# Kernel optimization log

Hardware: AMD Instinct MI355X
Metric: run time of the kernel (lower is better)

Reference implementation:

```python
import jax, jax.numpy as jnp
import numpy as np

B, T, I, H = 64, 2048, 64, 128


def setup_inputs() -> dict:
    key = jax.random.key(0)
    ks = jax.random.split(key, 6)
    std = 1.0 / np.sqrt(H)
    return {
        "x": jax.random.normal(ks[0], (B, T, I), dtype=jnp.float32),
        "h0": jax.random.normal(ks[1], (B, H), dtype=jnp.float32),
        "W": jax.random.uniform(ks[2], (H, I), dtype=jnp.float32, minval=-std, maxval=std),
        "U": jax.random.uniform(ks[3], (H, H), dtype=jnp.float32, minval=-std, maxval=std),
        "b_ih": jax.random.uniform(ks[4], (H,), dtype=jnp.float32, minval=-std, maxval=std),
        "b_hh": jax.random.uniform(ks[5], (H,), dtype=jnp.float32, minval=-std, maxval=std),
    }


def reference(x, h0, W, U, b_ih, b_hh):
    # Precompute the input projection for all timesteps in one big GEMM:
    # xw[b,t,h] = W x_t + b_ih + b_hh  (biases folded in once)
    xw = jnp.einsum("bti,hi->bth", x, W) + b_ih + b_hh  # [B,T,H]
    xw_t = jnp.swapaxes(xw, 0, 1)  # [T,B,H] for scan over time

    def step(h, xt):
        # vanilla tanh RNN cell: h' = tanh(W x + U h + b_ih + b_hh)
        h_new = jnp.tanh(xt + h @ U.T)
        return h_new, h_new

    h_last, ys = jax.lax.scan(step, h0, xw_t)  # ys: [T,B,H]
    output = jnp.swapaxes(ys, 0, 1)  # batch_first -> [B,T,H]
    return output, h_last
```

## Files before the change

kernel.cpp:

```cpp
#include <hip/hip_runtime.h>


#define RNN_B 64
#define RNN_T 2048
#define RNN_I 64
#define RNN_H 128
#define CH    32
#define NCH   (RNN_T / CH)

__device__ __forceinline__ float fast_tanh(float x) {
  float e = __builtin_amdgcn_exp2f(x * 2.885390081777927f);
  return 1.0f - 2.0f * __builtin_amdgcn_rcpf(e + 1.0f);
}

template <int CTRL>
__device__ __forceinline__ float dpp_add(float s) {
  int o = __builtin_amdgcn_mov_dpp(__float_as_int(s), CTRL, 0xF, 0xF, true);
  return s + __int_as_float(o);
}

__device__ __forceinline__ void fma4(float4& a, const float4 u, const float4 h) {
  a.x = fmaf(u.x, h.x, a.x);
  a.y = fmaf(u.y, h.y, a.y);
  a.z = fmaf(u.z, h.z, a.z);
  a.w = fmaf(u.w, h.w, a.w);
}

__device__ __forceinline__ float hsum(const float4 a) {
  return (a.x + a.y) + (a.z + a.w);
}

__device__ __forceinline__ void pin4(float4& v) {
  asm volatile("" : "+v"(v.x), "+v"(v.y), "+v"(v.z), "+v"(v.w));
}

__global__ __launch_bounds__(256, 2) void rnn_xw_gemm(
    const float* __restrict__ x, const float* __restrict__ W,
    const float* __restrict__ b_ih, const float* __restrict__ b_hh,
    float* __restrict__ xw) {
  const int tid = threadIdx.x;
  const int g   = tid >> 2;
  const int q   = tid & 3;

  float4 w[2][4];
#pragma unroll
  for (int r = 0; r < 2; ++r) {
    const float4* Wr = (const float4*)(W + (2 * g + r) * RNN_I + 16 * q);
#pragma unroll
    for (int m = 0; m < 4; ++m) { w[r][m] = Wr[m]; pin4(w[r][m]); }
  }
  const int row_own = 2 * g + (q & 1);
  const float bias  = b_ih[row_own] + b_hh[row_own];

  __shared__ __align__(16) float4 xs[64 * 16];
  const long rbase = (long)blockIdx.x * 64;
  const float4* xg = (const float4*)(x + rbase * RNN_I);
#pragma unroll
  for (int jj = 0; jj < 4; ++jj) xs[tid + 256 * jj] = xg[tid + 256 * jj];
  __syncthreads();

  for (int r = 0; r < 64; ++r) {
    const float4* xr = xs + r * 16 + q * 4;
    float4 a0 = {0, 0, 0, 0}, a1 = {0, 0, 0, 0};
#pragma unroll
    for (int m = 0; m < 4; ++m) {
      const float4 xv = xr[m];
      fma4(a0, w[0][m], xv);
      fma4(a1, w[1][m], xv);
    }
    float s0 = hsum(a0), s1 = hsum(a1);
    s0 = dpp_add<0xB1>(s0); s0 = dpp_add<0x4E>(s0);
    s1 = dpp_add<0xB1>(s1); s1 = dpp_add<0x4E>(s1);
    const float own = (q & 1) ? s1 : s0;
    if (q < 2)
      xw[(rbase + r) * RNN_H + row_own] = own + bias;
  }
}

__global__ __launch_bounds__(512, 2) void rnn_scan(
    const float* xw,
    float* out, float* __restrict__ hlast,
    const float* __restrict__ h0, const float* __restrict__ U) {
  const int b     = blockIdx.x;
  const int tid   = threadIdx.x;
  const int g     = tid >> 3;
  const int j     = tid & 7;
  const int r_own = 2 * g + (j & 1);

  __shared__ __align__(16) float hbuf0[8 * 20];
  __shared__ __align__(16) float hbuf1[8 * 20];
  __shared__ __align__(16) float xbuf[CH * RNN_H];
  __shared__ __align__(16) float obuf[CH * RNN_H];

  float4 u[2][4];
#pragma unroll
  for (int r = 0; r < 2; ++r) {
    const float4* Ur = (const float4*)(U + (2 * g + r) * RNN_H + 16 * j);
#pragma unroll
    for (int m = 0; m < 4; ++m) { u[r][m] = Ur[m]; pin4(u[r][m]); }
  }

  if (tid < RNN_H)
    hbuf0[(tid >> 4) * 20 + (tid & 15)] = h0[b * RNN_H + tid];

  const int hoff = (r_own >> 4) * 20 + (r_own & 15);
  const long base   = (long)b * RNN_T * RNN_H;
  const float4* xw4 = (const float4*)(xw + base);
  float4* out4      = (float4*)(out + base);
  float4* xb4       = (float4*)xbuf;
  const float4* ob4 = (const float4*)obuf;

  float4 p0 = xw4[tid], p1 = xw4[tid + 512];

  auto step = [&](const float* src, float* dst, int tc) {
    const float xv = xbuf[tc * RNN_H + r_own];
    const float4* hp = (const float4*)(src + 20 * j);
    float4 a0 = {0, 0, 0, 0}, a1 = {0, 0, 0, 0};
#pragma unroll
    for (int m = 0; m < 4; ++m) {
      const float4 hv = hp[m];
      fma4(a0, u[0][m], hv);
      fma4(a1, u[1][m], hv);
    }
    float s0 = hsum(a0), s1 = hsum(a1);
    s0 = dpp_add<0xB1>(s0); s0 = dpp_add<0x4E>(s0); s0 = dpp_add<0x141>(s0);
    s1 = dpp_add<0xB1>(s1); s1 = dpp_add<0x4E>(s1); s1 = dpp_add<0x141>(s1);
    const float own = (j & 1) ? s1 : s0;
    const float val = fast_tanh(own + xv);
    if (j < 2) {
      dst[hoff] = val;
    } else if ((j & 6) == 4) {
      obuf[tc * RNN_H + r_own] = val;
    }
    __syncthreads();
  };

  for (int c = 0; c < NCH; ++c) {
    xb4[tid] = p0; xb4[tid + 512] = p1;
    if (c + 1 < NCH) {
      const float4* nx = xw4 + (long)(c + 1) * 1024;
      p0 = nx[tid]; p1 = nx[tid + 512];
    }
    if (c > 0) {
      out4[(long)(c - 1) * 1024 + tid]       = ob4[tid];
      out4[(long)(c - 1) * 1024 + tid + 512] = ob4[tid + 512];
    }
    __syncthreads();

    for (int tc = 0; tc < CH; tc += 2) {
      step(hbuf0, hbuf1, tc);
      step(hbuf1, hbuf0, tc + 1);
    }
  }

  out4[(long)(NCH - 1) * 1024 + tid]       = ob4[tid];
  out4[(long)(NCH - 1) * 1024 + tid + 512] = ob4[tid + 512];
  if (tid < RNN_H)
    hlast[b * RNN_H + tid] = hbuf0[(tid >> 4) * 20 + (tid & 15)];
}

extern "C" void kernel_launch(void* const* d_in, const int* in_sizes, int n_in,
                              void* d_out, int out_size, void* d_ws, size_t ws_size,
                              hipStream_t stream) {
  const float* x    = (const float*)d_in[0];
  const float* h0   = (const float*)d_in[1];
  const float* W    = (const float*)d_in[2];
  const float* U    = (const float*)d_in[3];
  const float* b_ih = (const float*)d_in[4];
  const float* b_hh = (const float*)d_in[5];

  float* out   = (float*)d_out;
  float* hlast = out + (long)RNN_B * RNN_T * RNN_H;

  rnn_xw_gemm<<<(RNN_B * RNN_T) / 64, 256, 0, stream>>>(x, W, b_ih, b_hh, out);
  rnn_scan<<<RNN_B, 512, 0, stream>>>(out, out, hlast, h0, U);
}
```

Baseline: 800.8 us.

## Repartition RNN matvec to 4 rows x 8 columns per thread with 16-lane DPP reduction

Both kernels now give each thread 4 output rows and an 8-element column slice instead of 2 rows and 16 columns. Each step reads fewer LDS h values per thread, and the dot products use serial FMA chains. The cross-lane reduction grows to 4 DPP adds over 16 lanes for each of 4 partial sums. The scan also loads the next step's xw from shared memory ahead of the barrier to keep it off the critical path, and the padded h-buffer layout changes to fit the new read pattern. The trade is more DPP reduction work per step against shorter LDS reads and FMA chains.

```diff
diff --git a/kernel.cpp b/kernel.cpp
--- a/kernel.cpp
+++ b/kernel.cpp
@@ -19,19 +19,17 @@
   return s + __int_as_float(o);
 }
 
-__device__ __forceinline__ void fma4(float4& a, const float4 u, const float4 h) {
-  a.x = fmaf(u.x, h.x, a.x);
-  a.y = fmaf(u.y, h.y, a.y);
-  a.z = fmaf(u.z, h.z, a.z);
-  a.w = fmaf(u.w, h.w, a.w);
-}
-
-__device__ __forceinline__ float hsum(const float4 a) {
-  return (a.x + a.y) + (a.z + a.w);
-}
-
-__device__ __forceinline__ void pin4(float4& v) {
-  asm volatile("" : "+v"(v.x), "+v"(v.y), "+v"(v.z), "+v"(v.w));
+__device__ __forceinline__ float dot8(const float4 u0, const float4 u1,
+                                      const float4 h0, const float4 h1) {
+  float s = u0.x * h0.x;
+  s = fmaf(u0.y, h0.y, s);
+  s = fmaf(u0.z, h0.z, s);
+  s = fmaf(u0.w, h0.w, s);
+  s = fmaf(u1.x, h1.x, s);
+  s = fmaf(u1.y, h1.y, s);
+  s = fmaf(u1.z, h1.z, s);
+  s = fmaf(u1.w, h1.w, s);
+  return s;
 }
 
 __global__ __launch_bounds__(256, 2) void rnn_xw_gemm(
@@ -39,18 +37,18 @@
     const float* __restrict__ b_ih, const float* __restrict__ b_hh,
     float* __restrict__ xw) {
   const int tid = threadIdx.x;
-  const int g   = tid >> 2;
-  const int q   = tid & 3;
+  const int g   = tid >> 3;
+  const int c   = tid & 7;
+  const int r_own = 4 * g + (c & 3);
 
-  float4 w[2][4];
+  float4 w[4][2];
 #pragma unroll
-  for (int r = 0; r < 2; ++r) {
-    const float4* Wr = (const float4*)(W + (2 * g + r) * RNN_I + 16 * q);
-#pragma unroll
-    for (int m = 0; m < 4; ++m) { w[r][m] = Wr[m]; pin4(w[r][m]); }
+  for (int r = 0; r < 4; ++r) {
+    const float4* Wr = (const float4*)(W + (4 * g + r) * RNN_I + 8 * c);
+    w[r][0] = Wr[0];
+    w[r][1] = Wr[1];
   }
-  const int row_own = 2 * g + (q & 1);
-  const float bias  = b_ih[row_own] + b_hh[row_own];
+  const float bias = b_ih[r_own] + b_hh[r_own];
 
   __shared__ __align__(16) float4 xs[64 * 16];
   const long rbase = (long)blockIdx.x * 64;
@@ -60,20 +58,20 @@
   __syncthreads();
 
   for (int r = 0; r < 64; ++r) {
-    const float4* xr = xs + r * 16 + q * 4;
-    float4 a0 = {0, 0, 0, 0}, a1 = {0, 0, 0, 0};
-#pragma unroll
-    for (int m = 0; m < 4; ++m) {
-      const float4 xv = xr[m];
-      fma4(a0, w[0][m], xv);
-      fma4(a1, w[1][m], xv);
-    }
-    float s0 = hsum(a0), s1 = hsum(a1);
-    s0 = dpp_add<0xB1>(s0); s0 = dpp_add<0x4E>(s0);
-    s1 = dpp_add<0xB1>(s1); s1 = dpp_add<0x4E>(s1);
-    const float own = (q & 1) ? s1 : s0;
-    if (q < 2)
-      xw[(rbase + r) * RNN_H + row_own] = own + bias;
+    const float4* xr = xs + r * 16 + 2 * c;
+    const float4 hv0 = xr[0], hv1 = xr[1];
+    float s0 = dot8(w[0][0], w[0][1], hv0, hv1);
+    float s1 = dot8(w[1][0], w[1][1], hv0, hv1);
+    float s2 = dot8(w[2][0], w[2][1], hv0, hv1);
+    float s3 = dot8(w[3][0], w[3][1], hv0, hv1);
+    s0 = dpp_add<0xB1>(s0); s0 = dpp_add<0x4E>(s0); s0 = dpp_add<0x141>(s0);
+    s1 = dpp_add<0xB1>(s1); s1 = dpp_add<0x4E>(s1); s1 = dpp_add<0x141>(s1);
+    s2 = dpp_add<0xB1>(s2); s2 = dpp_add<0x4E>(s2); s2 = dpp_add<0x141>(s2);
+    s3 = dpp_add<0xB1>(s3); s3 = dpp_add<0x4E>(s3); s3 = dpp_add<0x141>(s3);
+    const float own = (c & 2) ? ((c & 1) ? s3 : s2)
+                              : ((c & 1) ? s1 : s0);
+    if (c < 4)
+      xw[(rbase + r) * RNN_H + r_own] = own + bias;
   }
 }
 
@@ -83,27 +81,28 @@
     const float* __restrict__ h0, const float* __restrict__ U) {
   const int b     = blockIdx.x;
   const int tid   = threadIdx.x;
-  const int g     = tid >> 3;
-  const int j     = tid & 7;
-  const int r_own = 2 * g + (j & 1);
+  const int g     = tid >> 4;
+  const int c     = tid & 15;
+  const int r_own = 4 * g + (c & 3);
 
-  __shared__ __align__(16) float hbuf0[8 * 20];
-  __shared__ __align__(16) float hbuf1[8 * 20];
+  __shared__ __align__(16) float hbuf0[140];
+  __shared__ __align__(16) float hbuf1[140];
   __shared__ __align__(16) float xbuf[CH * RNN_H];
   __shared__ __align__(16) float obuf[CH * RNN_H];
 
-  float4 u[2][4];
+  float4 u[4][2];
 #pragma unroll
-  for (int r = 0; r < 2; ++r) {
-    const float4* Ur = (const float4*)(U + (2 * g + r) * RNN_H + 16 * j);
-#pragma unroll
-    for (int m = 0; m < 4; ++m) { u[r][m] = Ur[m]; pin4(u[r][m]); }
+  for (int r = 0; r < 4; ++r) {
+    const float4* Ur = (const float4*)(U + (4 * g + r) * RNN_H + 8 * c);
+    u[r][0] = Ur[0];
+    u[r][1] = Ur[1];
   }
 
   if (tid < RNN_H)
-    hbuf0[(tid >> 4) * 20 + (tid & 15)] = h0[b * RNN_H + tid];
+    hbuf0[tid + 4 * (tid >> 5)] = h0[b * RNN_H + tid];
 
-  const int hoff = (r_own >> 4) * 20 + (r_own & 15);
+  const int hrd = 8 * c + 4 * (c >> 2);
+  const int hwr = r_own + 4 * (r_own >> 5);
   const long base   = (long)b * RNN_T * RNN_H;
   const float4* xw4 = (const float4*)(xw + base);
   float4* out4      = (float4*)(out + base);
@@ -112,41 +111,49 @@
 
   float4 p0 = xw4[tid], p1 = xw4[tid + 512];
 
+  float xv_cur;
+
   auto step = [&](const float* src, float* dst, int tc) {
-    const float xv = xbuf[tc * RNN_H + r_own];
-    const float4* hp = (const float4*)(src + 20 * j);
-    float4 a0 = {0, 0, 0, 0}, a1 = {0, 0, 0, 0};
-#pragma unroll
-    for (int m = 0; m < 4; ++m) {
-      const float4 hv = hp[m];
-      fma4(a0, u[0][m], hv);
-      fma4(a1, u[1][m], hv);
-    }
-    float s0 = hsum(a0), s1 = hsum(a1);
-    s0 = dpp_add<0xB1>(s0); s0 = dpp_add<0x4E>(s0); s0 = dpp_add<0x141>(s0);
-    s1 = dpp_add<0xB1>(s1); s1 = dpp_add<0x4E>(s1); s1 = dpp_add<0x141>(s1);
-    const float own = (j & 1) ? s1 : s0;
-    const float val = fast_tanh(own + xv);
-    if (j < 2) {
-      dst[hoff] = val;
-    } else if ((j & 6) == 4) {
+    const float4* hp = (const float4*)(src + hrd);
+    const float4 hv0 = hp[0], hv1 = hp[1];
+    float s0 = dot8(u[0][0], u[0][1], hv0, hv1);
+    float s1 = dot8(u[1][0], u[1][1], hv0, hv1);
+    float s2 = dot8(u[2][0], u[2][1], hv0, hv1);
+    float s3 = dot8(u[3][0], u[3][1], hv0, hv1);
+    const float xv_next = xbuf[((tc + 1) & (CH - 1)) * RNN_H + r_own];
+    s0 = dpp_add<0x121>(s0); s0 = dpp_add<0x122>(s0);
+    s0 = dpp_add<0x124>(s0); s0 = dpp_add<0x128>(s0);
+    s1 = dpp_add<0x121>(s1); s1 = dpp_add<0x122>(s1);
+    s1 = dpp_add<0x124>(s1); s1 = dpp_add<0x128>(s1);
+    s2 = dpp_add<0x121>(s2); s2 = dpp_add<0x122>(s2);
+    s2 = dpp_add<0x124>(s2); s2 = dpp_add<0x128>(s2);
+    s3 = dpp_add<0x121>(s3); s3 = dpp_add<0x122>(s3);
+    s3 = dpp_add<0x124>(s3); s3 = dpp_add<0x128>(s3);
+    const float own = (c & 2) ? ((c & 1) ? s3 : s2)
+                              : ((c & 1) ? s1 : s0);
+    const float val = fast_tanh(own + xv_cur);
+    if (c < 4) {
+      dst[hwr] = val;
+    } else if (c < 8) {
       obuf[tc * RNN_H + r_own] = val;
     }
     __syncthreads();
+    xv_cur = xv_next;
   };
 
-  for (int c = 0; c < NCH; ++c) {
+  for (int ch = 0; ch < NCH; ++ch) {
     xb4[tid] = p0; xb4[tid + 512] = p1;
-    if (c + 1 < NCH) {
-      const float4* nx = xw4 + (long)(c + 1) * 1024;
+    if (ch + 1 < NCH) {
+      const float4* nx = xw4 + (long)(ch + 1) * 1024;
       p0 = nx[tid]; p1 = nx[tid + 512];
     }
-    if (c > 0) {
-      out4[(long)(c - 1) * 1024 + tid]       = ob4[tid];
-      out4[(long)(c - 1) * 1024 + tid + 512] = ob4[tid + 512];
+    if (ch > 0) {
+      out4[(long)(ch - 1) * 1024 + tid]       = ob4[tid];
+      out4[(long)(ch - 1) * 1024 + tid + 512] = ob4[tid + 512];
     }
     __syncthreads();
 
+    xv_cur = xbuf[r_own];
     for (int tc = 0; tc < CH; tc += 2) {
       step(hbuf0, hbuf1, tc);
       step(hbuf1, hbuf0, tc + 1);
@@ -156,7 +163,7 @@
   out4[(long)(NCH - 1) * 1024 + tid]       = ob4[tid];
   out4[(long)(NCH - 1) * 1024 + tid + 512] = ob4[tid + 512];
   if (tid < RNN_H)
-    hlast[b * RNN_H + tid] = hbuf0[(tid >> 4) * 20 + (tid & 15)];
+    hlast[b * RNN_H + tid] = hbuf0[tid + 4 * (tid >> 5)];
 }
 
 extern "C" void kernel_launch(void* const* d_in, const int* in_sizes, int n_in,
```

Result: faster. 746.2 us (-6.8%).
